# Kernel tuning notes

Hardware: AMD Instinct MI355X
Metric: run time of the kernel (lower is better)

The kernel has to match this reference:

```python
import jax, jax.numpy as jnp
import numpy as np

B, L, E, H, D = 4, 4096, 1024, 16, 64  # batch, seq, embed, heads, head_dim
EPS = 1e-6


def setup_inputs() -> dict:
    key = jax.random.key(0)
    k1, k2, k3 = jax.random.split(key, 3)
    return {
        "q": jax.random.normal(k1, (B, L, E), dtype=jnp.float32),
        "k": jax.random.normal(k2, (B, L, E), dtype=jnp.float32),
        "v": jax.random.normal(k3, (B, L, E), dtype=jnp.float32),
        "mask": jnp.ones((B, L), dtype=jnp.float32),
    }


def _split_heads(x):
    # (B, L, E) -> (B*H, L, D)
    return x.reshape(B, L, H, D).transpose(0, 2, 1, 3).reshape(B * H, L, D)


def reference(q, k, v, mask):
    # feature map: relu
    q = jax.nn.relu(q)
    k = jax.nn.relu(k)
    # padding mask applied to keys/values
    k = k * mask[:, :, None]
    v = v * mask[:, :, None]
    q = _split_heads(q)
    k = _split_heads(k)
    v = _split_heads(v)
    # cosFormer sin/cos reweighting: pi/2 * i / m for i = 1..L
    idx = (np.pi / 2) * jnp.arange(1, L + 1, dtype=jnp.float32) / L
    s = jnp.sin(idx)[None, :, None]  # (1, L, 1)
    c = jnp.cos(idx)[None, :, None]
    q_ = jnp.concatenate([q * s, q * c], axis=-1)  # (B*H, L, 2D)
    k_ = jnp.concatenate([k * s, k * c], axis=-1)
    # linear-attention KV accumulation (non-causal): (B*H, 2D, D)
    kv = jnp.einsum('nld,nlm->ndm', k_, v)
    # normalizer
    z = 1.0 / jnp.maximum(jnp.einsum('nld,nd->nl', q_, k_.sum(axis=1)), EPS)
    out = jnp.einsum('nld,ndm,nl->nlm', q_, kv, z)  # (B*H, L, D)
    return out.reshape(B, H, L, D)
```

## Files before the change

kernel.cpp:

```cpp
#include <hip/hip_runtime.h>
#include <hip/hip_bf16.h>
#include <math.h>

#define B_ 4
#define L_ 4096
#define E_ 1024
#define H_ 16
#define D_ 64
#define N_ 64
#define D2_ 128
#define EPS_ 1e-6f

#define CH_ 16
#define LC_ (L_ / CH_)
#define LT2_ 32
#define NST_ (LC_ / LT2_)

#define DANG_ 3.83495197e-4f

typedef short short8 __attribute__((ext_vector_type(8)));
typedef float f32x4 __attribute__((ext_vector_type(4)));
typedef unsigned int u32;
typedef unsigned short u16;

static __device__ __forceinline__ u32 pack2bf(float a, float b) {
  union { __hip_bfloat16 h; u16 s; } x, y;
  x.h = __float2bfloat16(a);
  y.h = __float2bfloat16(b);
  return (u32)x.s | ((u32)y.s << 16);
}

static __device__ __forceinline__ short bf1(float a) {
  union { __hip_bfloat16 h; short s; } x;
  x.h = __float2bfloat16(a);
  return x.s;
}

static __device__ __forceinline__ void gld16(const void* g, void* l) {
  __builtin_amdgcn_global_load_lds(
      (const __attribute__((address_space(1))) unsigned int*)g,
      (__attribute__((address_space(3))) unsigned int*)l, 16, 0, 0);
}

#define BAR_() __builtin_amdgcn_s_barrier()
#define WAIT_LGKM0_()                                     \
  {                                                       \
    asm volatile("s_waitcnt lgkmcnt(0)" ::: "memory");    \
    __builtin_amdgcn_sched_barrier(0);                    \
  }
#define WAIT_VM4_()                                       \
  {                                                       \
    asm volatile("s_waitcnt vmcnt(4)" ::: "memory");      \
    __builtin_amdgcn_sched_barrier(0);                    \
  }
#define WAIT_VM0_()                                       \
  {                                                       \
    asm volatile("s_waitcnt vmcnt(0)" ::: "memory");      \
    __builtin_amdgcn_sched_barrier(0);                    \
  }

__global__ __launch_bounds__(256, 3) void phase1_mfma(
    const float* __restrict__ k, const float* __restrict__ v,
    const float* __restrict__ mask,
    float* __restrict__ part_kv, float* __restrict__ part_ks) {
  __shared__ __align__(16) float kraw[2][LT2_ * 64];
  __shared__ __align__(16) float vraw[2][LT2_ * 64];
  __shared__ __align__(16) u16 ka[D2_ * 40];
  __shared__ __align__(16) u16 vt[D_ * 40];
  __shared__ float msh[LC_];

  const int bid = blockIdx.x;
  const int n = bid & 63;
  const int ch = bid >> 6;
  const int b = n >> 4;
  const int h = n & 15;
  const int t = threadIdx.x;
  const int wv = t >> 6;
  const int lane = t & 63;
  const int c_lo = lane & 15;
  const int lp = lane >> 4;
  const int lp2 = t >> 4;
  const int dg = t & 15;
  const int l0 = ch * LC_;

  u32* ka32 = (u32*)ka;
  u32* vt32 = (u32*)vt;

  f32x4 acc[2][4];
#pragma unroll
  for (int i = 0; i < 2; ++i)
#pragma unroll
    for (int j = 0; j < 4; ++j) acc[i][j] = (f32x4)0.f;
  f32x4 acc5[2];
  acc5[0] = (f32x4)0.f;
  acc5[1] = (f32x4)0.f;

  short8 bones = {0, 0, 0, 0, 0, 0, 0, 0};
  if (c_lo == 0) {
#pragma unroll
    for (int j = 0; j < 8; ++j) bones[j] = (short)0x3F80;
  }

#define P1_GLD(S, BUF)                                                       \
  do {                                                                       \
    _Pragma("unroll") for (int j_ = 0; j_ < 2; ++j_) {                       \
      const int r32_ = 8 * wv + 4 * j_ + lp;                                 \
      const int lg_ = l0 + (S) * LT2_ + r32_;                                \
      const size_t gs_ = (size_t)(b * L_ + lg_) * E_ + h * 64;               \
      const int so_ = (c_lo ^ (r32_ & 15)) << 2;                             \
      gld16(k + gs_ + so_, &kraw[BUF][(8 * wv + 4 * j_) * 64]);              \
      gld16(v + gs_ + so_, &vraw[BUF][(8 * wv + 4 * j_) * 64]);              \
    }                                                                        \
  } while (0)

#define P1_PACK(BUF, S)                                                      \
  do {                                                                       \
    const int la_ = 2 * lp2, lb_ = la_ + 1;                                  \
    const float m0_ = msh[(S) * LT2_ + la_];                                 \
    const float m1_ = msh[(S) * LT2_ + lb_];                                 \
    const int lga_ = l0 + (S) * LT2_ + la_;                                  \
    float s0_, c0_, s1_, c1_;                                                \
    __sincosf((float)(lga_ + 1) * DANG_, &s0_, &c0_);                        \
    __sincosf((float)(lga_ + 2) * DANG_, &s1_, &c1_);                        \
    const int sa_ = la_ & 15, sb_ = lb_ & 15;                                \
    _Pragma("unroll") for (int dj_ = 0; dj_ < 4; ++dj_) {                    \
      const int d_ = dg + 16 * dj_;                                          \
      const int gl_ = d_ >> 2, su_ = d_ & 3;                                 \
      const float k0_ = kraw[BUF][la_ * 64 + ((gl_ ^ sa_) << 2) + su_];      \
      const float k1_ = kraw[BUF][lb_ * 64 + ((gl_ ^ sb_) << 2) + su_];      \
      const float v0_ = vraw[BUF][la_ * 64 + ((gl_ ^ sa_) << 2) + su_];      \
      const float v1_ = vraw[BUF][lb_ * 64 + ((gl_ ^ sb_) << 2) + su_];      \
      const float kr0_ = fmaxf(k0_, 0.f) * m0_;                              \
      const float kr1_ = fmaxf(k1_, 0.f) * m1_;                              \
      ka32[d_ * 20 + lp2] = pack2bf(kr0_ * s0_, kr1_ * s1_);                 \
      ka32[(d_ + 64) * 20 + lp2] = pack2bf(kr0_ * c0_, kr1_ * c1_);          \
      vt32[d_ * 20 + lp2] = pack2bf(v0_ * m0_, v1_ * m1_);                   \
    }                                                                        \
  } while (0)

#define P1_MMA()                                                             \
  do {                                                                       \
    short8 af_[2], bf_[4];                                                   \
    _Pragma("unroll") for (int dt_ = 0; dt_ < 2; ++dt_)                      \
        af_[dt_] = *(const short8*)&ka[(wv * 32 + dt_ * 16 + c_lo) * 40 +    \
                                       lp * 8];                              \
    _Pragma("unroll") for (int mt_ = 0; mt_ < 4; ++mt_)                      \
        bf_[mt_] = *(const short8*)&vt[(mt_ * 16 + c_lo) * 40 + lp * 8];     \
    _Pragma("unroll") for (int dt_ = 0; dt_ < 2; ++dt_) {                    \
      _Pragma("unroll") for (int mt_ = 0; mt_ < 4; ++mt_)                    \
          acc[dt_][mt_] = __builtin_amdgcn_mfma_f32_16x16x32_bf16(           \
              af_[dt_], bf_[mt_], acc[dt_][mt_], 0, 0, 0);                   \
      acc5[dt_] = __builtin_amdgcn_mfma_f32_16x16x32_bf16(af_[dt_], bones,   \
                                                          acc5[dt_], 0, 0,   \
                                                          0);                \
    }                                                                        \
  } while (0)

#define P1_STEP(S, BUF)                                                      \
  do {                                                                       \
    P1_PACK(BUF, S);                                                         \
    WAIT_LGKM0_();                                                           \
    BAR_();                                                                  \
    P1_MMA();                                                                \
    P1_GLD((S) + 2, BUF);                                                    \
    WAIT_VM4_();                                                             \
    BAR_();                                                                  \
  } while (0)

  if (wv == 0) gld16(mask + (size_t)b * L_ + l0 + lane * 4, msh);
  P1_GLD(0, 0);
  P1_GLD(1, 1);
  WAIT_VM4_();
  BAR_();

  P1_STEP(0, 0);
  P1_STEP(1, 1);
  P1_STEP(2, 0);
  P1_STEP(3, 1);
  P1_STEP(4, 0);
  P1_STEP(5, 1);
  P1_PACK(0, 6);
  WAIT_LGKM0_();
  BAR_();
  P1_MMA();
  WAIT_VM0_();
  BAR_();
  P1_PACK(1, 7);
  WAIT_LGKM0_();
  BAR_();
  P1_MMA();

  const size_t pbase = (size_t)(ch * N_ + n) * (D2_ * D_);
#pragma unroll
  for (int dt = 0; dt < 2; ++dt) {
    const int d = wv * 32 + dt * 16 + lp * 4;
#pragma unroll
    for (int mt = 0; mt < 4; ++mt) {
      const int mcol = mt * 16 + c_lo;
#pragma unroll
      for (int r = 0; r < 4; ++r)
        part_kv[pbase + (size_t)(d + r) * D_ + mcol] = acc[dt][mt][r];
    }
  }
  if (c_lo == 0) {
#pragma unroll
    for (int dt = 0; dt < 2; ++dt)
#pragma unroll
      for (int r = 0; r < 4; ++r)
        part_ks[(size_t)(ch * N_ + n) * D2_ + wv * 32 + dt * 16 + lp * 4 + r] =
            acc5[dt][r];
  }
}

__global__ __launch_bounds__(256) void reduce_t(
    const float* __restrict__ part_kv, const float* __restrict__ part_ks,
    u16* __restrict__ kvt, float* __restrict__ ks) {
  __shared__ __align__(16) float tsh[16 * 68];
  const int bid = blockIdx.x;
  const int n = bid >> 3;
  const int sl = bid & 7;
  const int t = threadIdx.x;

  const int e0 = sl * 1024 + t * 4;
  f32x4 s = (f32x4)0.f;
#pragma unroll
  for (int cc = 0; cc < CH_; ++cc)
    s += *(const f32x4*)&part_kv[(size_t)(cc * N_ + n) * (D2_ * D_) + e0];
  *(f32x4*)&tsh[(t >> 4) * 68 + (t & 15) * 4] = s;

  if (sl == 0 && t < D2_) {
    float ss = 0.f;
#pragma unroll
    for (int cc = 0; cc < CH_; ++cc)
      ss += part_ks[(size_t)(cc * N_ + n) * D2_ + t];
    ks[n * D2_ + t] = ss;
  }
  __syncthreads();

  const int m = t >> 2;
  const int d4 = (t & 3) * 4;
  const u32 lo = pack2bf(tsh[(d4 + 0) * 68 + m], tsh[(d4 + 1) * 68 + m]);
  const u32 hi = pack2bf(tsh[(d4 + 2) * 68 + m], tsh[(d4 + 3) * 68 + m]);
  uint2 pk; pk.x = lo; pk.y = hi;
  *(uint2*)&kvt[(size_t)n * (D2_ * D_) + (size_t)m * D2_ + sl * 16 + d4] = pk;
}

__global__ __launch_bounds__(256, 3) void phase2_mfma(
    const float* __restrict__ q, const u16* __restrict__ kvt,
    const float* __restrict__ ks, float* __restrict__ out) {
  __shared__ __align__(16) float qsh[2 * 64 * 64];
  __shared__ __align__(16) u16 kbsh[64 * 128];

  const int bid = blockIdx.x;
  const int n = bid & 63;
  const int g2 = bid >> 6;
  const int b = n >> 4, h = n & 15;
  const int t = threadIdx.x;
  const int wv = t >> 6, lane = t & 63;
  const int c_lo = lane & 15, quad = lane >> 4;
  const int l0 = g2 * 128;

  const float* qbase = q + (size_t)(b * L_ + l0) * E_ + h * 64;
  const u16* kvbase = kvt + (size_t)n * (D2_ * D_);
  const int rsub = lane >> 4;
  const int g = lane & 15;
#pragma unroll
  for (int j = 0; j < 4; ++j) {
    const int r = wv * 16 + j * 4 + rsub;
    const int sw = (g ^ (r & 15));
    gld16(kvbase + (size_t)r * D2_ + (sw << 3),
          kbsh + (wv * 16 + j * 4) * 128);
    gld16(qbase + (size_t)r * E_ + (sw << 2),
          qsh + (wv * 16 + j * 4) * 64);
    gld16(qbase + (size_t)(64 + r) * E_ + (sw << 2),
          qsh + 4096 + (wv * 16 + j * 4) * 64);
  }

  const float* ksn = ks + n * D2_;
  short8 bks[4];
#pragma unroll
  for (int kk = 0; kk < 4; ++kk) {
    const f32x4 ka_ = *(const f32x4*)(ksn + kk * 32 + quad * 8);
    const f32x4 kb_ = *(const f32x4*)(ksn + kk * 32 + quad * 8 + 4);
    short8 tt = {0, 0, 0, 0, 0, 0, 0, 0};
    if (c_lo == 0) {
#pragma unroll
      for (int j = 0; j < 4; ++j) {
        tt[j] = bf1(ka_[j]);
        tt[j + 4] = bf1(kb_[j]);
      }
    }
    bks[kk] = tt;
  }

  __syncthreads();

#pragma unroll
  for (int cc = 0; cc < 2; ++cc) {
    const int row = wv * 16 + c_lo;
    const int glr = l0 + cc * 64 + row;
    float sv, cv;
    __sincosf((float)(glr + 1) * DANG_, &sv, &cv);

    const float* qrow = qsh + cc * 4096 + row * 64;
    const int sw = row & 15;
    const f32x4 a0 = *(const f32x4*)(qrow + (((2 * quad) ^ sw) << 2));
    const f32x4 a1 = *(const f32x4*)(qrow + (((2 * quad + 1) ^ sw) << 2));
    const f32x4 a2 = *(const f32x4*)(qrow + (((8 + 2 * quad) ^ sw) << 2));
    const f32x4 a3 = *(const f32x4*)(qrow + (((9 + 2 * quad) ^ sw) << 2));

    short8 af[4];
#pragma unroll
    for (int j = 0; j < 4; ++j) {
      const float x0 = fmaxf(a0[j], 0.f);
      const float x1 = fmaxf(a1[j], 0.f);
      const float x2 = fmaxf(a2[j], 0.f);
      const float x3 = fmaxf(a3[j], 0.f);
      af[0][j] = bf1(x0 * sv); af[0][j + 4] = bf1(x1 * sv);
      af[1][j] = bf1(x2 * sv); af[1][j + 4] = bf1(x3 * sv);
      af[2][j] = bf1(x0 * cv); af[2][j + 4] = bf1(x1 * cv);
      af[3][j] = bf1(x2 * cv); af[3][j + 4] = bf1(x3 * cv);
    }

    f32x4 acc[4];
#pragma unroll
    for (int mt = 0; mt < 4; ++mt) acc[mt] = (f32x4)0.f;
    f32x4 acc5 = (f32x4)0.f;

#pragma unroll
    for (int kk = 0; kk < 4; ++kk) {
#pragma unroll
      for (int mt = 0; mt < 4; ++mt) {
        const int m = mt * 16 + c_lo;
        const short8 bfr = *(const short8*)
            &kbsh[m * 128 + (((kk * 4 + quad) ^ (m & 15)) << 3)];
        acc[mt] =
            __builtin_amdgcn_mfma_f32_16x16x32_bf16(af[kk], bfr, acc[mt], 0, 0, 0);
      }
      acc5 = __builtin_amdgcn_mfma_f32_16x16x32_bf16(af[kk], bks[kk], acc5, 0, 0, 0);
    }

#pragma unroll
    for (int r = 0; r < 4; ++r) {
      const float den = __shfl(acc5[r], quad * 16);
      const float z = 1.f / fmaxf(den, EPS_);
      const int gl = l0 + cc * 64 + wv * 16 + quad * 4 + r;
      const size_t ob = (size_t)n * (L_ * D_) + (size_t)gl * D_;
#pragma unroll
      for (int mt = 0; mt < 4; ++mt)
        out[ob + mt * 16 + c_lo] = acc[mt][r] * z;
    }
  }
}

extern "C" void kernel_launch(void* const* d_in, const int* in_sizes, int n_in,
                              void* d_out, int out_size, void* d_ws,
                              size_t ws_size, hipStream_t stream) {
  const float* q = (const float*)d_in[0];
  const float* k = (const float*)d_in[1];
  const float* v = (const float*)d_in[2];
  const float* mask = (const float*)d_in[3];
  float* out = (float*)d_out;

  float* part_kv = (float*)d_ws;
  float* part_ks = part_kv + (size_t)CH_ * N_ * D2_ * D_;
  u16* kvt = (u16*)(part_ks + (size_t)CH_ * N_ * D2_);
  float* ks = (float*)(kvt + (size_t)N_ * D2_ * D_);

  phase1_mfma<<<dim3(CH_ * N_), dim3(256), 0, stream>>>(k, v, mask, part_kv, part_ks);
  reduce_t<<<dim3(N_ * 8), dim3(256), 0, stream>>>(part_kv, part_ks, kvt, ks);
  phase2_mfma<<<dim3(N_ * 32), dim3(256), 0, stream>>>(q, kvt, ks, out);
}
```

Baseline: 247.0 us.

## Process two heads per phase1 block with triple-buffered 16-row loads

Phase1 now has each block handle two adjacent heads, loading 512-byte row segments (128 columns) instead of 256-byte ones. Loads are triple-buffered in 16-row stages, and the bf16 pack buffers are double-buffered so two stages are packed per barrier group before the MMAs run. The aim is wider, more coalesced global reads and more memory-level parallelism per block. In exchange the grid is halved to 512 blocks, the accumulator register count doubles, and launch bounds drop to 2 blocks per SM, so occupancy falls.

```diff
diff --git a/kernel.cpp b/kernel.cpp
--- a/kernel.cpp
+++ b/kernel.cpp
@@ -13,8 +13,8 @@
 
 #define CH_ 16
 #define LC_ (L_ / CH_)
-#define LT2_ 32
-#define NST_ (LC_ / LT2_)
+#define ST_ 16
+#define NSTG_ 16
 
 #define DANG_ 3.83495197e-4f
 
@@ -59,41 +59,49 @@
     __builtin_amdgcn_sched_barrier(0);                    \
   }
 
-__global__ __launch_bounds__(256, 3) void phase1_mfma(
+__global__ __launch_bounds__(256, 2) void phase1_mfma(
     const float* __restrict__ k, const float* __restrict__ v,
     const float* __restrict__ mask,
     float* __restrict__ part_kv, float* __restrict__ part_ks) {
-  __shared__ __align__(16) float kraw[2][LT2_ * 64];
-  __shared__ __align__(16) float vraw[2][LT2_ * 64];
-  __shared__ __align__(16) u16 ka[D2_ * 40];
-  __shared__ __align__(16) u16 vt[D_ * 40];
+  __shared__ __align__(16) float kraw[3][ST_ * 128];
+  __shared__ __align__(16) float vraw[3][ST_ * 128];
+  __shared__ __align__(16) u16 ka[2][D2_ * 36];
+  __shared__ __align__(16) u16 vt[2][D_ * 36];
   __shared__ float msh[LC_];
 
   const int bid = blockIdx.x;
-  const int n = bid & 63;
-  const int ch = bid >> 6;
-  const int b = n >> 4;
-  const int h = n & 15;
+  const int p = bid & 31;
+  const int ch = bid >> 5;
+  const int b = p >> 3;
+  const int hcol0 = (p & 7) * 128;
   const int t = threadIdx.x;
   const int wv = t >> 6;
   const int lane = t & 63;
   const int c_lo = lane & 15;
   const int lp = lane >> 4;
-  const int lp2 = t >> 4;
-  const int dg = t & 15;
   const int l0 = ch * LC_;
+
+  const int hh = t >> 7;
+  const int tt = t & 127;
+  const int lp2h = tt >> 4;
+  const int dg = tt & 15;
 
   u32* ka32 = (u32*)ka;
   u32* vt32 = (u32*)vt;
 
-  f32x4 acc[2][4];
-#pragma unroll
-  for (int i = 0; i < 2; ++i)
-#pragma unroll
-    for (int j = 0; j < 4; ++j) acc[i][j] = (f32x4)0.f;
-  f32x4 acc5[2];
-  acc5[0] = (f32x4)0.f;
-  acc5[1] = (f32x4)0.f;
+  f32x4 acc[2][2][4];
+#pragma unroll
+  for (int hq = 0; hq < 2; ++hq)
+#pragma unroll
+    for (int i = 0; i < 2; ++i)
+#pragma unroll
+      for (int j = 0; j < 4; ++j) acc[hq][i][j] = (f32x4)0.f;
+  f32x4 acc5[2][2];
+#pragma unroll
+  for (int hq = 0; hq < 2; ++hq) {
+    acc5[hq][0] = (f32x4)0.f;
+    acc5[hq][1] = (f32x4)0.f;
+  }
 
   short8 bones = {0, 0, 0, 0, 0, 0, 0, 0};
   if (c_lo == 0) {
@@ -104,111 +112,117 @@
 #define P1_GLD(S, BUF)                                                       \
   do {                                                                       \
     _Pragma("unroll") for (int j_ = 0; j_ < 2; ++j_) {                       \
-      const int r32_ = 8 * wv + 4 * j_ + lp;                                 \
-      const int lg_ = l0 + (S) * LT2_ + r32_;                                \
-      const size_t gs_ = (size_t)(b * L_ + lg_) * E_ + h * 64;               \
-      const int so_ = (c_lo ^ (r32_ & 15)) << 2;                             \
-      gld16(k + gs_ + so_, &kraw[BUF][(8 * wv + 4 * j_) * 64]);              \
-      gld16(v + gs_ + so_, &vraw[BUF][(8 * wv + 4 * j_) * 64]);              \
+      const int jr_ = 4 * wv + 2 * j_;                                       \
+      const int r_ = jr_ + (lane >> 5);                                      \
+      const int g_ = lane & 31;                                              \
+      const size_t gs_ = (size_t)(b * L_ + l0 + (S) * ST_ + r_) * E_ +       \
+                         hcol0 + ((g_ ^ r_) << 2);                           \
+      gld16(k + gs_, &kraw[BUF][jr_ * 128]);                                 \
+      gld16(v + gs_, &vraw[BUF][jr_ * 128]);                                 \
     }                                                                        \
   } while (0)
 
-#define P1_PACK(BUF, S)                                                      \
+#define P1_PACK(S, BUF)                                                      \
   do {                                                                       \
-    const int la_ = 2 * lp2, lb_ = la_ + 1;                                  \
-    const float m0_ = msh[(S) * LT2_ + la_];                                 \
-    const float m1_ = msh[(S) * LT2_ + lb_];                                 \
-    const int lga_ = l0 + (S) * LT2_ + la_;                                  \
+    const int la_ = 2 * lp2h, lb_ = la_ + 1;                                 \
+    const float m0_ = msh[(S) * ST_ + la_];                                  \
+    const float m1_ = msh[(S) * ST_ + lb_];                                  \
+    const int lga_ = l0 + (S) * ST_ + la_;                                   \
     float s0_, c0_, s1_, c1_;                                                \
     __sincosf((float)(lga_ + 1) * DANG_, &s0_, &c0_);                        \
     __sincosf((float)(lga_ + 2) * DANG_, &s1_, &c1_);                        \
-    const int sa_ = la_ & 15, sb_ = lb_ & 15;                                \
+    const int li_ = ((S) & 1) * 8 + lp2h;                                    \
     _Pragma("unroll") for (int dj_ = 0; dj_ < 4; ++dj_) {                    \
       const int d_ = dg + 16 * dj_;                                          \
-      const int gl_ = d_ >> 2, su_ = d_ & 3;                                 \
-      const float k0_ = kraw[BUF][la_ * 64 + ((gl_ ^ sa_) << 2) + su_];      \
-      const float k1_ = kraw[BUF][lb_ * 64 + ((gl_ ^ sb_) << 2) + su_];      \
-      const float v0_ = vraw[BUF][la_ * 64 + ((gl_ ^ sa_) << 2) + su_];      \
-      const float v1_ = vraw[BUF][lb_ * 64 + ((gl_ ^ sb_) << 2) + su_];      \
+      const int c_ = hh * 64 + d_;                                           \
+      const int G_ = c_ >> 2, su_ = c_ & 3;                                  \
+      const float k0_ = kraw[BUF][la_ * 128 + ((G_ ^ la_) << 2) + su_];      \
+      const float k1_ = kraw[BUF][lb_ * 128 + ((G_ ^ lb_) << 2) + su_];      \
+      const float v0_ = vraw[BUF][la_ * 128 + ((G_ ^ la_) << 2) + su_];      \
+      const float v1_ = vraw[BUF][lb_ * 128 + ((G_ ^ lb_) << 2) + su_];      \
       const float kr0_ = fmaxf(k0_, 0.f) * m0_;                              \
       const float kr1_ = fmaxf(k1_, 0.f) * m1_;                              \
-      ka32[d_ * 20 + lp2] = pack2bf(kr0_ * s0_, kr1_ * s1_);                 \
-      ka32[(d_ + 64) * 20 + lp2] = pack2bf(kr0_ * c0_, kr1_ * c1_);          \
-      vt32[d_ * 20 + lp2] = pack2bf(v0_ * m0_, v1_ * m1_);                   \
+      ka32[hh * (D2_ * 18) + d_ * 18 + li_] = pack2bf(kr0_ * s0_, kr1_ * s1_); \
+      ka32[hh * (D2_ * 18) + (d_ + 64) * 18 + li_] =                         \
+          pack2bf(kr0_ * c0_, kr1_ * c1_);                                   \
+      vt32[hh * (D_ * 18) + d_ * 18 + li_] = pack2bf(v0_ * m0_, v1_ * m1_);  \
     }                                                                        \
   } while (0)
 
 #define P1_MMA()                                                             \
   do {                                                                       \
-    short8 af_[2], bf_[4];                                                   \
-    _Pragma("unroll") for (int dt_ = 0; dt_ < 2; ++dt_)                      \
-        af_[dt_] = *(const short8*)&ka[(wv * 32 + dt_ * 16 + c_lo) * 40 +    \
-                                       lp * 8];                              \
-    _Pragma("unroll") for (int mt_ = 0; mt_ < 4; ++mt_)                      \
-        bf_[mt_] = *(const short8*)&vt[(mt_ * 16 + c_lo) * 40 + lp * 8];     \
-    _Pragma("unroll") for (int dt_ = 0; dt_ < 2; ++dt_) {                    \
+    _Pragma("unroll") for (int hq_ = 0; hq_ < 2; ++hq_) {                    \
+      short8 af_[2], bf_[4];                                                 \
+      _Pragma("unroll") for (int dt_ = 0; dt_ < 2; ++dt_)                    \
+          af_[dt_] = *(const short8*)&ka[hq_][(wv * 32 + dt_ * 16 + c_lo) *  \
+                                                 36 + lp * 8];               \
       _Pragma("unroll") for (int mt_ = 0; mt_ < 4; ++mt_)                    \
-          acc[dt_][mt_] = __builtin_amdgcn_mfma_f32_16x16x32_bf16(           \
-              af_[dt_], bf_[mt_], acc[dt_][mt_], 0, 0, 0);                   \
-      acc5[dt_] = __builtin_amdgcn_mfma_f32_16x16x32_bf16(af_[dt_], bones,   \
-                                                          acc5[dt_], 0, 0,   \
-                                                          0);                \
+          bf_[mt_] = *(const short8*)&vt[hq_][(mt_ * 16 + c_lo) * 36 +       \
+                                              lp * 8];                       \
+      _Pragma("unroll") for (int dt_ = 0; dt_ < 2; ++dt_) {                  \
+        _Pragma("unroll") for (int mt_ = 0; mt_ < 4; ++mt_)                  \
+            acc[hq_][dt_][mt_] = __builtin_amdgcn_mfma_f32_16x16x32_bf16(    \
+                af_[dt_], bf_[mt_], acc[hq_][dt_][mt_], 0, 0, 0);            \
+        acc5[hq_][dt_] = __builtin_amdgcn_mfma_f32_16x16x32_bf16(            \
+            af_[dt_], bones, acc5[hq_][dt_], 0, 0, 0);                       \
+      }                                                                      \
     }                                                                        \
   } while (0)
 
-#define P1_STEP(S, BUF)                                                      \
+#define P1_GROUP(S, I3, I4, VMN)                                             \
   do {                                                                       \
-    P1_PACK(BUF, S);                                                         \
+    P1_PACK((S), (S) % 3);                                                   \
+    BAR_();                           \
+    if (I3) P1_GLD((S) + 3, (S) % 3);                                        \
+    P1_PACK((S) + 1, ((S) + 1) % 3);                                         \
     WAIT_LGKM0_();                                                           \
-    BAR_();                                                                  \
+    BAR_();                                              \
+    if (I4) P1_GLD((S) + 4, ((S) + 1) % 3);                                  \
     P1_MMA();                                                                \
-    P1_GLD((S) + 2, BUF);                                                    \
-    WAIT_VM4_();                                                             \
-    BAR_();                                                                  \
+    if ((VMN) == 4) { WAIT_VM4_(); }                                         \
+    else if ((VMN) == 0) { WAIT_VM0_(); }                                    \
+    BAR_();                             \
   } while (0)
 
   if (wv == 0) gld16(mask + (size_t)b * L_ + l0 + lane * 4, msh);
   P1_GLD(0, 0);
   P1_GLD(1, 1);
+  P1_GLD(2, 2);
   WAIT_VM4_();
   BAR_();
 
-  P1_STEP(0, 0);
-  P1_STEP(1, 1);
-  P1_STEP(2, 0);
-  P1_STEP(3, 1);
-  P1_STEP(4, 0);
-  P1_STEP(5, 1);
-  P1_PACK(0, 6);
-  WAIT_LGKM0_();
-  BAR_();
-  P1_MMA();
-  WAIT_VM0_();
-  BAR_();
-  P1_PACK(1, 7);
-  WAIT_LGKM0_();
-  BAR_();
-  P1_MMA();
-
-  const size_t pbase = (size_t)(ch * N_ + n) * (D2_ * D_);
-#pragma unroll
-  for (int dt = 0; dt < 2; ++dt) {
-    const int d = wv * 32 + dt * 16 + lp * 4;
-#pragma unroll
-    for (int mt = 0; mt < 4; ++mt) {
-      const int mcol = mt * 16 + c_lo;
-#pragma unroll
-      for (int r = 0; r < 4; ++r)
-        part_kv[pbase + (size_t)(d + r) * D_ + mcol] = acc[dt][mt][r];
-    }
-  }
-  if (c_lo == 0) {
-#pragma unroll
-    for (int dt = 0; dt < 2; ++dt)
-#pragma unroll
-      for (int r = 0; r < 4; ++r)
-        part_ks[(size_t)(ch * N_ + n) * D2_ + wv * 32 + dt * 16 + lp * 4 + r] =
-            acc5[dt][r];
+  P1_GROUP(0, 1, 1, 4);
+  P1_GROUP(2, 1, 1, 4);
+  P1_GROUP(4, 1, 1, 4);
+  P1_GROUP(6, 1, 1, 4);
+  P1_GROUP(8, 1, 1, 4);
+  P1_GROUP(10, 1, 1, 4);
+  P1_GROUP(12, 1, 0, 0);
+  P1_GROUP(14, 0, 0, -1);
+
+#pragma unroll
+  for (int hq = 0; hq < 2; ++hq) {
+    const int n = 2 * p + hq;
+    const size_t pbase = (size_t)(ch * N_ + n) * (D2_ * D_);
+#pragma unroll
+    for (int dt = 0; dt < 2; ++dt) {
+      const int d = wv * 32 + dt * 16 + lp * 4;
+#pragma unroll
+      for (int mt = 0; mt < 4; ++mt) {
+        const int mcol = mt * 16 + c_lo;
+#pragma unroll
+        for (int r = 0; r < 4; ++r)
+          part_kv[pbase + (size_t)(d + r) * D_ + mcol] = acc[hq][dt][mt][r];
+      }
+    }
+    if (c_lo == 0) {
+#pragma unroll
+      for (int dt = 0; dt < 2; ++dt)
+#pragma unroll
+        for (int r = 0; r < 4; ++r)
+          part_ks[(size_t)(ch * N_ + n) * D2_ + wv * 32 + dt * 16 + lp * 4 +
+                  r] = acc5[hq][dt][r];
+    }
   }
 }
 
@@ -367,7 +381,7 @@
   u16* kvt = (u16*)(part_ks + (size_t)CH_ * N_ * D2_);
   float* ks = (float*)(kvt + (size_t)N_ * D2_ * D_);
 
-  phase1_mfma<<<dim3(CH_ * N_), dim3(256), 0, stream>>>(k, v, mask, part_kv, part_ks);
+  phase1_mfma<<<dim3(CH_ * 32), dim3(256), 0, stream>>>(k, v, mask, part_kv, part_ks);
   reduce_t<<<dim3(N_ * 8), dim3(256), 0, stream>>>(part_kv, part_ks, kvt, ks);
   phase2_mfma<<<dim3(N_ * 32), dim3(256), 0, stream>>>(q, kvt, ks, out);
 }
```

Result: faster. 238.9 us (-3.3%).
